# Kernel tuning notes

Measured on AMD Instinct MI355X. Metric: run time of the kernel, lower is better.

## Reference

```python
import jax, jax.numpy as jnp
import numpy as np

B, S, DM, H = 4, 1024, 1024, 16
D = DM // H  # attn_head_size = 64


def setup_inputs() -> dict:
    key = jax.random.key(0)
    ks = jax.random.split(key, 16)
    sc = 0.02
    return {
        "hidden_states": jax.random.normal(ks[0], (B, S, DM), jnp.float32),
        "wq": jax.random.normal(ks[1], (DM, DM), jnp.float32) * sc,
        "bq": jax.random.normal(ks[2], (DM,), jnp.float32) * sc,
        "wk": jax.random.normal(ks[3], (DM, DM), jnp.float32) * sc,
        "bk": jax.random.normal(ks[4], (DM,), jnp.float32) * sc,
        "wv": jax.random.normal(ks[5], (DM, DM), jnp.float32) * sc,
        "bv": jax.random.normal(ks[6], (DM,), jnp.float32) * sc,
        "wo": jax.random.normal(ks[7], (DM, DM), jnp.float32) * sc,
        "bo": jax.random.normal(ks[8], (DM,), jnp.float32) * sc,
        "wfq": jax.random.normal(ks[9], (DM, DM), jnp.float32) * sc,
        "bfq": jax.random.normal(ks[10], (DM,), jnp.float32) * sc,
        "wfg": jax.random.normal(ks[11], (DM, DM), jnp.float32) * sc,
        "bfg": jax.random.normal(ks[12], (DM,), jnp.float32) * sc,
        "up": jax.random.normal(ks[13], (H, 1, D), jnp.float32) * sc,
        "uz": jax.random.normal(ks[14], (H, 1, D), jnp.float32) * sc,
    }


def _split_heads(x):
    # [B, S, DM] -> [B, H, S, D]
    return x.reshape(x.shape[0], x.shape[1], H, D).transpose(0, 2, 1, 3)


def reference(hidden_states, wq, bq, wk, bk, wv, bv, wo, bo,
              wfq, bfq, wfg, bfg, up, uz):
    key_len = hidden_states.shape[1]
    mixed_q = hidden_states @ wq + bq  # [B, S, DM]
    mixed_k = hidden_states @ wk + bk
    mixed_v = hidden_states @ wv + bv

    # focus-attention Gaussian bias
    glo = jnp.mean(mixed_q, axis=1, keepdims=True)                      # [B, 1, DM]
    c = jnp.tanh((mixed_q @ wfq + bfq) + (glo @ wfg + bfg))             # [B, S, DM]
    c = _split_heads(c)                                                 # [B, H, S, D]
    p = jnp.sum(c * up[None], axis=-1)                                  # [B, H, S]
    z = jnp.sum(c * uz[None], axis=-1)                                  # [B, H, S]
    P = jax.nn.sigmoid(p) * key_len                                     # [B, H, S]
    Z = jax.nn.sigmoid(z) * key_len
    j = jnp.arange(key_len, dtype=P.dtype)                              # [S]
    # G[b,h,q,k] = -(k - P[b,h,q])^2 * 2 / Z[b,h,q]^2
    G = -((j[None, None, None, :] - P[..., None]) ** 2) * 2.0 / (Z[..., None] ** 2)

    q = _split_heads(mixed_q)
    k = _split_heads(mixed_k)
    v = _split_heads(mixed_v)

    scores = jnp.einsum("bhqd,bhkd->bhqk", q, k) / jnp.sqrt(jnp.float32(D))
    scores = scores + G
    probs = jax.nn.softmax(scores, axis=-1)  # dropout_prob = 0 -> no-op
    ctx = jnp.einsum("bhqk,bhkd->bhqd", probs, v)
    ctx = ctx.transpose(0, 2, 1, 3).reshape(ctx.shape[0], key_len, H * D)
    return ctx @ wo + bo
```

## Files before the change

kernel.cpp:

```cpp
#include <hip/hip_runtime.h>
#include <hip/hip_bf16.h>
#include <stdint.h>

#define DEV __device__ __forceinline__

typedef __attribute__((ext_vector_type(4))) float f32x4;
typedef __attribute__((ext_vector_type(8))) __bf16 bf16x8;
typedef __attribute__((ext_vector_type(4))) __bf16 bf16x4;
typedef __attribute__((ext_vector_type(4))) unsigned int uint4v;
typedef __attribute__((ext_vector_type(4))) int i32x4;

static constexpr int Bc = 4, Sc = 1024, DMc = 1024, Hc = 16, Dh = 64;
static constexpr int Mc = Bc * Sc;

DEV __bf16 f2b(float x) {
    unsigned u = __builtin_bit_cast(unsigned, x);
    unsigned r = (u + 0x7fffu + ((u >> 16) & 1u)) >> 16;
    return __builtin_bit_cast(__bf16, (unsigned short)r);
}
DEV float b2f(__bf16 x) {
    unsigned short s = __builtin_bit_cast(unsigned short, x);
    unsigned u = ((unsigned)s) << 16;
    return __builtin_bit_cast(float, u);
}
DEV unsigned cvt_pk_bf16(float a, float b) {
    unsigned r;
    asm("v_cvt_pk_bf16_f32 %0, %1, %2" : "=v"(r) : "v"(a), "v"(b));
    return r;
}
DEV void gload_lds16(const void* g, void* l) {
    __builtin_amdgcn_global_load_lds(
        (const __attribute__((address_space(1))) unsigned int*)g,
        (__attribute__((address_space(3))) unsigned int*)l,
        16, 0, 0);
}
DEV bf16x8 ldswz(const __bf16* base, int row, int cu) {
    const char* p = (const char*)base + row * 128 + (((cu) ^ (row & 7)) << 4);
    return *(const bf16x8*)p;
}

__global__ void k_cvt2(const float* __restrict__ hs, __bf16* __restrict__ hsb,
                       float* __restrict__ part0) {
    int sc = blockIdx.x, b = blockIdx.y, tid = threadIdx.x;
    int c0 = tid * 4;
    float4 s = {0.f, 0.f, 0.f, 0.f};
#pragma unroll
    for (int r = 0; r < 8; r++) {
        size_t row = (size_t)b * 1024 + sc * 8 + r;
        float4 v = *(const float4*)&hs[row * 1024 + c0];
        s.x += v.x; s.y += v.y; s.z += v.z; s.w += v.w;
        bf16x4 o = { f2b(v.x), f2b(v.y), f2b(v.z), f2b(v.w) };
        *(bf16x4*)&hsb[row * 1024 + c0] = o;
    }
    *(float4*)&part0[(size_t)(sc * 4 + b) * 1024 + c0] = s;
}

__global__ void k_tcvt5(const float* __restrict__ s0, const float* __restrict__ s1,
                        const float* __restrict__ s2, const float* __restrict__ s3,
                        const float* __restrict__ s4,
                        __bf16* __restrict__ d0, __bf16* __restrict__ d1,
                        __bf16* __restrict__ d2, __bf16* __restrict__ d3,
                        __bf16* __restrict__ d4, __bf16* __restrict__ wqb) {
    __shared__ float t[32][33];
    const float* in; __bf16* out;
    switch (blockIdx.z) {
        case 0: in = s0; out = d0; break;
        case 1: in = s1; out = d1; break;
        case 2: in = s2; out = d2; break;
        case 3: in = s3; out = d3; break;
        default: in = s4; out = d4; break;
    }
    int c0 = blockIdx.x * 32, r0 = blockIdx.y * 32;
    for (int j = 0; j < 4; j++) {
        float v = in[(size_t)(r0 + threadIdx.y + j * 8) * 1024 + c0 + threadIdx.x];
        t[threadIdx.y + j * 8][threadIdx.x] = v;
        if (blockIdx.z == 0)
            wqb[(size_t)(r0 + threadIdx.y + j * 8) * 1024 + c0 + threadIdx.x] = f2b(v);
    }
    __syncthreads();
    for (int j = 0; j < 4; j++)
        out[(size_t)(c0 + threadIdx.y + j * 8) * 1024 + r0 + threadIdx.x] = f2b(t[threadIdx.x][threadIdx.y + j * 8]);
}

template <int EPI, int BM>
__global__ __launch_bounds__(256) void k_gemm(
    const __bf16* __restrict__ A, const __bf16* __restrict__ Bt,
    const float* __restrict__ bias, void* __restrict__ Cout, int N, int K)
{
    constexpr int MF = BM / 32;
    constexpr int ACH = BM / 32;
    __shared__ __bf16 Al[2][BM * 64];
    __shared__ __bf16 Bl[2][128 * 64];
    const int bm = blockIdx.x, bn = blockIdx.y;
    const int tid = threadIdx.x, lane = tid & 63, wid = tid >> 6;
    const int l15 = lane & 15, lg = lane >> 4;
    const int qr = (wid >> 1) * (BM / 2), qc = (wid & 1) * 64;
    f32x4 acc[MF][4] = {};

    const __bf16* Ab = A + (size_t)bm * BM * K;
    const __bf16* Bb = Bt + (size_t)bn * 128 * K;

#pragma unroll
    for (int c = 0; c < ACH; c++) {
        int ch = c * 256 + tid, row = ch >> 3, cu = (ch & 7) ^ (row & 7);
        gload_lds16(&Ab[(size_t)row * K + cu * 8], &Al[0][ch * 8]);
    }
#pragma unroll
    for (int c = 0; c < 4; c++) {
        int ch = c * 256 + tid, row = ch >> 3, cu = (ch & 7) ^ (row & 7);
        gload_lds16(&Bb[(size_t)row * K + cu * 8], &Bl[0][ch * 8]);
    }
    asm volatile("s_waitcnt vmcnt(0)" ::: "memory");
    __builtin_amdgcn_s_barrier();

    int buf = 0;
    for (int t = 0; t < K / 64; t++) {
        if (t + 1 < K / 64) {
            int k0 = (t + 1) * 64;
#pragma unroll
            for (int c = 0; c < ACH; c++) {
                int ch = c * 256 + tid, row = ch >> 3, cu = (ch & 7) ^ (row & 7);
                gload_lds16(&Ab[(size_t)row * K + k0 + cu * 8], &Al[buf ^ 1][ch * 8]);
            }
#pragma unroll
            for (int c = 0; c < 4; c++) {
                int ch = c * 256 + tid, row = ch >> 3, cu = (ch & 7) ^ (row & 7);
                gload_lds16(&Bb[(size_t)row * K + k0 + cu * 8], &Bl[buf ^ 1][ch * 8]);
            }
        }
        bf16x8 af[MF][2], bfv[4][2];
#pragma unroll
        for (int m = 0; m < MF; m++)
#pragma unroll
            for (int ks = 0; ks < 2; ks++) af[m][ks] = ldswz(&Al[buf][0], qr + m * 16 + l15, ks * 4 + lg);
#pragma unroll
        for (int n = 0; n < 4; n++)
#pragma unroll
            for (int ks = 0; ks < 2; ks++) bfv[n][ks] = ldswz(&Bl[buf][0], qc + n * 16 + l15, ks * 4 + lg);
#pragma unroll
        for (int m = 0; m < MF; m++)
#pragma unroll
            for (int n = 0; n < 4; n++) {
                acc[m][n] = __builtin_amdgcn_mfma_f32_16x16x32_bf16(af[m][0], bfv[n][0], acc[m][n], 0, 0, 0);
                acc[m][n] = __builtin_amdgcn_mfma_f32_16x16x32_bf16(af[m][1], bfv[n][1], acc[m][n], 0, 0, 0);
            }
        asm volatile("s_waitcnt vmcnt(0)" ::: "memory");
        __builtin_amdgcn_s_barrier();
        buf ^= 1;
    }
#pragma unroll
    for (int m = 0; m < MF; m++) {
        int row_base = bm * BM + qr + m * 16 + lg * 4;
#pragma unroll
        for (int n = 0; n < 4; n++) {
            int col = bn * 128 + qc + n * 16 + l15;
            float bsum = bias ? bias[col] : 0.0f;
#pragma unroll
            for (int r = 0; r < 4; r++) {
                int row = row_base + r;
                float v = acc[m][n][r] + bsum;
                if constexpr (EPI == 2) ((float*)Cout)[(size_t)row * N + col] = v;
                else ((__bf16*)Cout)[(size_t)row * N + col] = f2b(v);
            }
        }
    }
}

__global__ __launch_bounds__(256) void k_qkvc(
    const __bf16* __restrict__ A, const __bf16* __restrict__ BtAll,
    const float* __restrict__ bq, const float* __restrict__ bk, const float* __restrict__ bv,
    const float* __restrict__ gt2, const float* __restrict__ up, const float* __restrict__ uz,
    __bf16* __restrict__ mq, __bf16* __restrict__ mk_, __bf16* __restrict__ mv_,
    float* __restrict__ Pf, float* __restrict__ Zf)
{
    constexpr int K = 1024;
    __shared__ __bf16 Al[2][128 * 64];
    __shared__ __bf16 Bl[2][128 * 64];
    const int bm = blockIdx.x, bn = blockIdx.y;
    const int tid = threadIdx.x, lane = tid & 63, wid = tid >> 6;
    const int l15 = lane & 15, lg = lane >> 4;
    const int qr = (wid >> 1) * 64, qc = (wid & 1) * 64;
    f32x4 acc[4][4] = {};

    const __bf16* Ab = A + (size_t)bm * 128 * K;
    const __bf16* Bb = BtAll + (size_t)bn * 128 * K;

#pragma unroll
    for (int c = 0; c < 4; c++) {
        int ch = c * 256 + tid, row = ch >> 3, cu = (ch & 7) ^ (row & 7);
        gload_lds16(&Ab[(size_t)row * K + cu * 8], &Al[0][ch * 8]);
        gload_lds16(&Bb[(size_t)row * K + cu * 8], &Bl[0][ch * 8]);
    }
    asm volatile("s_waitcnt vmcnt(0)" ::: "memory");
    __builtin_amdgcn_s_barrier();

    int buf = 0;
    for (int t = 0; t < 16; t++) {
        if (t < 15) {
            int k0 = (t + 1) * 64;
#pragma unroll
            for (int c = 0; c < 4; c++) {
                int ch = c * 256 + tid, row = ch >> 3, cu = (ch & 7) ^ (row & 7);
                gload_lds16(&Ab[(size_t)row * K + k0 + cu * 8], &Al[buf ^ 1][ch * 8]);
                gload_lds16(&Bb[(size_t)row * K + k0 + cu * 8], &Bl[buf ^ 1][ch * 8]);
            }
        }
        bf16x8 af[4][2], bfv[4][2];
#pragma unroll
        for (int m = 0; m < 4; m++)
#pragma unroll
            for (int ks = 0; ks < 2; ks++) af[m][ks] = ldswz(&Al[buf][0], qr + m * 16 + l15, ks * 4 + lg);
#pragma unroll
        for (int n = 0; n < 4; n++)
#pragma unroll
            for (int ks = 0; ks < 2; ks++) bfv[n][ks] = ldswz(&Bl[buf][0], qc + n * 16 + l15, ks * 4 + lg);
#pragma unroll
        for (int m = 0; m < 4; m++)
#pragma unroll
            for (int n = 0; n < 4; n++) {
                acc[m][n] = __builtin_amdgcn_mfma_f32_16x16x32_bf16(af[m][0], bfv[n][0], acc[m][n], 0, 0, 0);
                acc[m][n] = __builtin_amdgcn_mfma_f32_16x16x32_bf16(af[m][1], bfv[n][1], acc[m][n], 0, 0, 0);
            }
        asm volatile("s_waitcnt vmcnt(0)" ::: "memory");
        __builtin_amdgcn_s_barrier();
        buf ^= 1;
    }

    const int chunk = bn >> 3;
    if (chunk == 3) {
        const int h = (bn & 7) * 2 + (qc >> 6);
        float upv[4], uzv[4];
#pragma unroll
        for (int n = 0; n < 4; n++) {
            upv[n] = up[h * 64 + n * 16 + l15];
            uzv[n] = uz[h * 64 + n * 16 + l15];
        }
#pragma unroll
        for (int m = 0; m < 4; m++) {
            int row_base = bm * 128 + qr + m * 16 + lg * 4;
#pragma unroll
            for (int r = 0; r < 4; r++) {
                int row = row_base + r;
                float p = 0.f, z = 0.f;
#pragma unroll
                for (int n = 0; n < 4; n++) {
                    int col = (bn & 7) * 128 + qc + n * 16 + l15;
                    float cv = tanhf(acc[m][n][r] + gt2[(row >> 10) * 1024 + col]);
                    p += cv * upv[n];
                    z += cv * uzv[n];
                }
#pragma unroll
                for (int d = 1; d < 16; d <<= 1) {
                    p += __shfl_xor(p, d, 16);
                    z += __shfl_xor(z, d, 16);
                }
                if (l15 == 0) {
                    int bb = row >> 10, s = row & 1023;
                    Pf[((size_t)(bb * 16 + h)) * 1024 + s] = 1024.f / (1.f + __expf(-p));
                    Zf[((size_t)(bb * 16 + h)) * 1024 + s] = 1024.f / (1.f + __expf(-z));
                }
            }
        }
    } else {
        const float* bias = chunk == 0 ? bq : chunk == 1 ? bk : bv;
        __bf16* outp = chunk == 0 ? mq : chunk == 1 ? mk_ : mv_;
#pragma unroll
        for (int m = 0; m < 4; m++) {
            int row_base = bm * 128 + qr + m * 16 + lg * 4;
#pragma unroll
            for (int n = 0; n < 4; n++) {
                int col = (bn & 7) * 128 + qc + n * 16 + l15;
                float bsum = bias[col];
#pragma unroll
                for (int r = 0; r < 4; r++) {
                    int row = row_base + r;
                    outp[(size_t)row * 1024 + col] = f2b(acc[m][n][r] + bsum);
                }
            }
        }
    }
}

__global__ void k_glo2(const float* __restrict__ part0, const float* __restrict__ wq,
                       float* __restrict__ glo_part) {
    __shared__ float ghs_l[256];
    int tid = threadIdx.x, kc = blockIdx.y;
    {
        int bb = tid >> 6, kk = tid & 63, k = kc * 64 + kk;
        float s = 0.f;
        for (int sc = 0; sc < 128; sc++) s += part0[(size_t)(sc * 4 + bb) * 1024 + k];
        ghs_l[tid] = s * (1.0f / 1024.f);
    }
    __syncthreads();
    int n = blockIdx.x * 256 + tid;
    float a0 = 0, a1 = 0, a2 = 0, a3 = 0;
    for (int j = 0; j < 64; j++) {
        float w = wq[(size_t)(kc * 64 + j) * 1024 + n];
        a0 += ghs_l[j] * w; a1 += ghs_l[64 + j] * w; a2 += ghs_l[128 + j] * w; a3 += ghs_l[192 + j] * w;
    }
    glo_part[(kc * 4 + 0) * 1024 + n] = a0;
    glo_part[(kc * 4 + 1) * 1024 + n] = a1;
    glo_part[(kc * 4 + 2) * 1024 + n] = a2;
    glo_part[(kc * 4 + 3) * 1024 + n] = a3;
}
__global__ void k_gt2p(const float* __restrict__ glo_part, const float* __restrict__ bq,
                       const float* __restrict__ wfg, const float* __restrict__ wfq,
                       float* __restrict__ gt_part) {
    __shared__ float glo_l[256];
    int tid = threadIdx.x, kc = blockIdx.y;
    {
        int bb = tid >> 6, kk = tid & 63, k = kc * 64 + kk;
        float s = bq[k];
        for (int k2 = 0; k2 < 16; k2++) s += glo_part[(k2 * 4 + bb) * 1024 + k];
        glo_l[tid] = s;
    }
    __syncthreads();
    int n = blockIdx.x * 256 + tid;
    float a0 = 0, a1 = 0, a2 = 0, a3 = 0, t = 0;
    for (int j = 0; j < 64; j++) {
        int k = kc * 64 + j;
        float wg = wfg[(size_t)k * 1024 + n];
        float wf = wfq[(size_t)k * 1024 + n];
        a0 += glo_l[j] * wg; a1 += glo_l[64 + j] * wg; a2 += glo_l[128 + j] * wg; a3 += glo_l[192 + j] * wg;
        t += bq[k] * wf;
    }
    gt_part[(kc * 4 + 0) * 1024 + n] = a0 + t;
    gt_part[(kc * 4 + 1) * 1024 + n] = a1 + t;
    gt_part[(kc * 4 + 2) * 1024 + n] = a2 + t;
    gt_part[(kc * 4 + 3) * 1024 + n] = a3 + t;
}
__global__ void k_red_gt(const float* __restrict__ gt_part, const float* __restrict__ bfg,
                         const float* __restrict__ bfq, float* __restrict__ gt2) {
    int i = blockIdx.x * 256 + threadIdx.x;
    int b = i >> 10, n = i & 1023;
    float s = bfg[n] + bfq[n];
    for (int kc = 0; kc < 16; kc++) s += gt_part[(kc * 4 + b) * 1024 + n];
    gt2[i] = s;
}

__global__ __launch_bounds__(256) void k_vt(const __bf16* __restrict__ mv_, __bf16* __restrict__ vt) {
    __shared__ __bf16 tl[64][72];
    int sc = blockIdx.x, h = blockIdx.y, b = blockIdx.z;
    int tid = threadIdx.x;
#pragma unroll
    for (int i = 0; i < 2; i++) {
        int ch = i * 256 + tid, srow = ch >> 3, off = ch & 7;
        bf16x8 v = *(const bf16x8*)&mv_[((size_t)(b * 1024 + sc * 64 + srow)) * 1024 + h * 64 + off * 8];
        *(bf16x8*)&tl[srow][off * 8] = v;
    }
    __syncthreads();
#pragma unroll
    for (int i = 0; i < 2; i++) {
        int ch = i * 256 + tid, d = ch >> 3, offs = ch & 7;
        bf16x8 o;
#pragma unroll
        for (int j = 0; j < 8; j++) o[j] = tl[offs * 8 + j][d];
        *(bf16x8*)&vt[((size_t)((b * 16 + h) * 64 + d)) * 1024 + sc * 64 + offs * 8] = o;
    }
}

DEV bf16x8 ldfrag(const __bf16* base, int row, int colbyte) {
    const char* p = (const char*)base + (size_t)row * 128 + (colbyte ^ ((row & 7) << 4));
    return *(const bf16x8*)p;
}

__global__ __launch_bounds__(256) void k_attn(
    const __bf16* __restrict__ Q, const __bf16* __restrict__ Kx, const __bf16* __restrict__ Vt_g,
    const float* __restrict__ Pf, const float* __restrict__ Zf, __bf16* __restrict__ ctx)
{
    __shared__ __bf16 Kl[2][64 * 64];
    __shared__ __bf16 Vl[2][64 * 64];
    const int qt = blockIdx.x, h = blockIdx.y, b = blockIdx.z;
    const int tid = threadIdx.x, lane = tid & 63, wid = tid >> 6;
    const int l15 = lane & 15, lg = lane >> 4;
    const int qbase = qt * 128 + wid * 32;
    const size_t qoff = ((size_t)(b * Sc)) * DMc + h * Dh;

    bf16x8 qf[2][2];
#pragma unroll
    for (int qh = 0; qh < 2; qh++)
#pragma unroll
        for (int dh = 0; dh < 2; dh++)
            qf[qh][dh] = *(const bf16x8*)&Q[qoff + (size_t)(qbase + qh * 16 + l15) * DMc + dh * 32 + lg * 8];

    float Pr[2], Ar[2];
#pragma unroll
    for (int qh = 0; qh < 2; qh++) {
        int row = qbase + qh * 16 + l15;
        float pp = Pf[((size_t)(b * 16 + h)) * 1024 + row];
        float zz = Zf[((size_t)(b * 16 + h)) * 1024 + row];
        Pr[qh] = pp; Ar[qh] = 2.0f / (zz * zz);
    }
    float m[2] = {-1e30f, -1e30f}, l[2] = {0.f, 0.f};
    f32x4 oacc[2][4] = {};

    const __bf16* Kbase = Kx + qoff;
    const __bf16* Vbase = Vt_g + ((size_t)((b * 16 + h) * 64)) * 1024;

#pragma unroll
    for (int i = 0; i < 2; i++) {
        int ch = i * 256 + tid, row = ch >> 3, off = ch & 7;
        uint4v kv = *(const uint4v*)&Kbase[(size_t)row * DMc + off * 8];
        uint4v vv = *(const uint4v*)&Vbase[(size_t)row * 1024 + off * 8];
        *(uint4v*)((char*)&Kl[0][0] + row * 128 + ((off * 16) ^ ((row & 7) << 4))) = kv;
        *(uint4v*)((char*)&Vl[0][0] + row * 128 + ((off * 16) ^ ((row & 7) << 4))) = vv;
    }
    __syncthreads();

    for (int t = 0; t < 16; t++) {
        const int buf = t & 1;
        uint4v rk[2], rv[2];
        if (t < 15) {
#pragma unroll
            for (int i = 0; i < 2; i++) {
                int ch = i * 256 + tid, row = ch >> 3, off = ch & 7;
                rk[i] = *(const uint4v*)&Kbase[(size_t)((t + 1) * 64 + row) * DMc + off * 8];
                rv[i] = *(const uint4v*)&Vbase[(size_t)row * 1024 + (t + 1) * 64 + off * 8];
            }
        }

        f32x4 st[2][4];
        __builtin_amdgcn_s_setprio(1);
#pragma unroll
        for (int c = 0; c < 4; c++) {
            bf16x8 kb0 = ldfrag(&Kl[buf][0], c * 16 + l15, lg * 16);
            bf16x8 kb1 = ldfrag(&Kl[buf][0], c * 16 + l15, 64 + lg * 16);
#pragma unroll
            for (int qh = 0; qh < 2; qh++) {
                f32x4 a = {0.f, 0.f, 0.f, 0.f};
                a = __builtin_amdgcn_mfma_f32_16x16x32_bf16(kb0, qf[qh][0], a, 0, 0, 0);
                a = __builtin_amdgcn_mfma_f32_16x16x32_bf16(kb1, qf[qh][1], a, 0, 0, 0);
                st[qh][c] = a;
            }
        }
        __builtin_amdgcn_s_setprio(0);

        int pk[2][4][2];
#pragma unroll
        for (int qh = 0; qh < 2; qh++) {
            float s[16];
            float mx = -1e30f;
#pragma unroll
            for (int c = 0; c < 4; c++)
#pragma unroll
                for (int r = 0; r < 4; r++) {
                    float kidx = (float)(t * 64 + c * 16 + lg * 4 + r);
                    float dk = kidx - Pr[qh];
                    float v = st[qh][c][r] * 0.125f - dk * dk * Ar[qh];
                    s[c * 4 + r] = v;
                    mx = fmaxf(mx, v);
                }
            mx = fmaxf(mx, __shfl_xor(mx, 16, 64));
            mx = fmaxf(mx, __shfl_xor(mx, 32, 64));
            float nm = fmaxf(m[qh], mx);
            float sc_ = __expf(m[qh] - nm);
            m[qh] = nm;
            float rs = 0.f;
#pragma unroll
            for (int i = 0; i < 16; i++) { float p = __expf(s[i] - nm); s[i] = p; rs += p; }
            rs += __shfl_xor(rs, 16, 64);
            rs += __shfl_xor(rs, 32, 64);
            l[qh] = l[qh] * sc_ + rs;
#pragma unroll
            for (int c = 0; c < 4; c++) {
                pk[qh][c][0] = (int)cvt_pk_bf16(s[c * 4 + 0], s[c * 4 + 1]);
                pk[qh][c][1] = (int)cvt_pk_bf16(s[c * 4 + 2], s[c * 4 + 3]);
            }
#pragma unroll
            for (int r = 0; r < 4; r++) {
                float scr = __shfl(sc_, lg * 4 + r, 16);
#pragma unroll
                for (int dt = 0; dt < 4; dt++) oacc[qh][dt][r] *= scr;
            }
        }

        const int a0 = (((lg & 1) << 1) * 16 + l15) * 4;
        const int a1 = a0 + 64;
        const int selhi = lg >> 1;
#pragma unroll
        for (int kh = 0; kh < 2; kh++) {
            bf16x8 vb[4];
#pragma unroll
            for (int dt = 0; dt < 4; dt++) vb[dt] = ldfrag(&Vl[buf][0], dt * 16 + l15, kh * 64 + lg * 16);
#pragma unroll
            for (int qh = 0; qh < 2; qh++) {
                int w[4];
#pragma unroll
                for (int wi = 0; wi < 4; wi++) {
                    int addr = (wi < 2) ? a0 : a1;
                    int pr = wi & 1;
                    int va = __builtin_amdgcn_ds_bpermute(addr, pk[qh][kh * 2 + 0][pr]);
                    int vb2 = __builtin_amdgcn_ds_bpermute(addr, pk[qh][kh * 2 + 1][pr]);
                    w[wi] = selhi ? vb2 : va;
                }
                i32x4 wv = {w[0], w[1], w[2], w[3]};
                bf16x8 pa = __builtin_bit_cast(bf16x8, wv);
                __builtin_amdgcn_s_setprio(1);
#pragma unroll
                for (int dt = 0; dt < 4; dt++)
                    oacc[qh][dt] = __builtin_amdgcn_mfma_f32_16x16x32_bf16(pa, vb[dt], oacc[qh][dt], 0, 0, 0);
                __builtin_amdgcn_s_setprio(0);
            }
        }

        if (t < 15) {
#pragma unroll
            for (int i = 0; i < 2; i++) {
                int ch = i * 256 + tid, row = ch >> 3, off = ch & 7;
                *(uint4v*)((char*)&Kl[buf ^ 1][0] + row * 128 + ((off * 16) ^ ((row & 7) << 4))) = rk[i];
                *(uint4v*)((char*)&Vl[buf ^ 1][0] + row * 128 + ((off * 16) ^ ((row & 7) << 4))) = rv[i];
            }
        }
        __syncthreads();
    }

#pragma unroll
    for (int qh = 0; qh < 2; qh++) {
        float lr[4];
#pragma unroll
        for (int r = 0; r < 4; r++) lr[r] = __shfl(l[qh], lg * 4 + r, 16);
#pragma unroll
        for (int dt = 0; dt < 4; dt++)
#pragma unroll
            for (int r = 0; r < 4; r++) {
                int row = qbase + qh * 16 + lg * 4 + r;
                ctx[((size_t)(b * Sc) + row) * DMc + h * Dh + dt * 16 + l15] =
                    f2b(oacc[qh][dt][r] / lr[r]);
            }
    }
}

extern "C" void kernel_launch(void* const* d_in, const int* in_sizes, int n_in,
                              void* d_out, int out_size, void* d_ws, size_t ws_size,
                              hipStream_t stream) {
    const float* hs  = (const float*)d_in[0];
    const float* wq  = (const float*)d_in[1];
    const float* bq  = (const float*)d_in[2];
    const float* wk  = (const float*)d_in[3];
    const float* bk  = (const float*)d_in[4];
    const float* wv  = (const float*)d_in[5];
    const float* bv  = (const float*)d_in[6];
    const float* wo  = (const float*)d_in[7];
    const float* bo  = (const float*)d_in[8];
    const float* wfq = (const float*)d_in[9];
    const float* bfq = (const float*)d_in[10];
    const float* wfg = (const float*)d_in[11];
    const float* bfg = (const float*)d_in[12];
    const float* up  = (const float*)d_in[13];
    const float* uz  = (const float*)d_in[14];

    char* ws = (char*)d_ws;
    const size_t MB = 1ull << 20;
    __bf16* hsb   = (__bf16*)(ws);
    __bf16* BtAll = (__bf16*)(ws + 8 * MB);
    __bf16* wfqT  = (__bf16*)(ws + 16 * MB);
    __bf16* woT   = (__bf16*)(ws + 18 * MB);
    __bf16* mq    = (__bf16*)(ws + 20 * MB);
    __bf16* mk    = (__bf16*)(ws + 28 * MB);
    __bf16* mv    = (__bf16*)(ws + 36 * MB);
    __bf16* vt    = (__bf16*)(ws + 44 * MB);
    __bf16* ctxb  = (__bf16*)(ws);
    __bf16* wqb   = (__bf16*)(ws + 55 * MB);
    char* sm = ws + 52 * MB;
    float* Pf       = (float*)(sm);
    float* Zf       = (float*)(sm + (256 << 10));
    float* glo_part = (float*)(sm + (512 << 10));
    float* gt_part  = (float*)(sm + (768 << 10));
    float* gt2      = (float*)(sm + (1024 << 10));
    float* part0    = (float*)(ws + 57 * MB);

    k_cvt2<<<dim3(128, 4), 256, 0, stream>>>(hs, hsb, part0);
    k_tcvt5<<<dim3(32, 32, 5), dim3(32, 8), 0, stream>>>(
        wq, wk, wv, wfq, wo,
        BtAll, BtAll + 1048576, BtAll + 2097152, wfqT, woT, wqb);

    k_glo2<<<dim3(4, 16), 256, 0, stream>>>(part0, wq, glo_part);
    k_gt2p<<<dim3(4, 16), 256, 0, stream>>>(glo_part, bq, wfg, wfq, gt_part);
    k_red_gt<<<16, 256, 0, stream>>>(gt_part, bfg, bfq, gt2);

    k_gemm<0, 64><<<dim3(16, 8), 256, 0, stream>>>(wfqT, wqb, nullptr, BtAll + 3145728, DMc, DMc);

    k_qkvc<<<dim3(32, 32), 256, 0, stream>>>(hsb, BtAll, bq, bk, bv, gt2, up, uz,
                                             mq, mk, mv, Pf, Zf);

    k_vt<<<dim3(16, 16, 4), 256, 0, stream>>>(mv, vt);

    k_attn<<<dim3(8, 16, 4), 256, 0, stream>>>(mq, mk, vt, Pf, Zf, ctxb);

    k_gemm<2, 64><<<dim3(64, 8), 256, 0, stream>>>(ctxb, woT, bo, d_out, DMc, DMc);
}
```

Before: 180.3 us.

## Fuse V transpose into QKV GEMM epilogue and halve GEMM K-tile to 32

The QKV GEMM epilogue now writes the V chunk directly in transposed [b,h,d,s] layout, which removes the separate k_vt transpose kernel and its global round trip through the mv buffer. Separately, both GEMM kernels switch from 64-wide to 32-wide K stages with a new 4-unit XOR swizzle. This halves LDS per block, which may raise occupancy, but doubles the number of barrier/wait iterations. The transposed stores are 8-byte strided writes, which may coalesce poorly.

Measured after the change: 193.1 us. +7.1%, slower.

```diff
diff --git a/kernel.cpp b/kernel.cpp
--- a/kernel.cpp
+++ b/kernel.cpp
@@ -34,8 +34,8 @@
         (__attribute__((address_space(3))) unsigned int*)l,
         16, 0, 0);
 }
-DEV bf16x8 ldswz(const __bf16* base, int row, int cu) {
-    const char* p = (const char*)base + row * 128 + (((cu) ^ (row & 7)) << 4);
+DEV bf16x8 ldswz32(const __bf16* base, int row, int lg) {
+    const char* p = (const char*)base + row * 64 + (((lg) ^ ((row >> 1) & 3)) << 4);
     return *(const bf16x8*)p;
 }
 
@@ -88,9 +88,9 @@
     const float* __restrict__ bias, void* __restrict__ Cout, int N, int K)
 {
     constexpr int MF = BM / 32;
-    constexpr int ACH = BM / 32;
-    __shared__ __bf16 Al[2][BM * 64];
-    __shared__ __bf16 Bl[2][128 * 64];
+    constexpr int ACH = BM / 64;
+    __shared__ __bf16 Al[2][BM * 32];
+    __shared__ __bf16 Bl[2][128 * 32];
     const int bm = blockIdx.x, bn = blockIdx.y;
     const int tid = threadIdx.x, lane = tid & 63, wid = tid >> 6;
     const int l15 = lane & 15, lg = lane >> 4;
@@ -100,54 +100,42 @@
     const __bf16* Ab = A + (size_t)bm * BM * K;
     const __bf16* Bb = Bt + (size_t)bn * 128 * K;
 
-#pragma unroll
-    for (int c = 0; c < ACH; c++) {
-        int ch = c * 256 + tid, row = ch >> 3, cu = (ch & 7) ^ (row & 7);
-        gload_lds16(&Ab[(size_t)row * K + cu * 8], &Al[0][ch * 8]);
-    }
-#pragma unroll
-    for (int c = 0; c < 4; c++) {
-        int ch = c * 256 + tid, row = ch >> 3, cu = (ch & 7) ^ (row & 7);
-        gload_lds16(&Bb[(size_t)row * K + cu * 8], &Bl[0][ch * 8]);
-    }
+#define STAGE_G(k0, dst)                                                          \
+    _Pragma("unroll")                                                             \
+    for (int c = 0; c < ACH; c++) {                                               \
+        int ch = c * 256 + tid, row = ch >> 2, u = ch & 3;                        \
+        int su = u ^ ((row >> 1) & 3);                                            \
+        gload_lds16(&Ab[(size_t)row * K + (k0) + su * 8], &Al[dst][ch * 8]);      \
+    }                                                                             \
+    _Pragma("unroll")                                                             \
+    for (int c = 0; c < 2; c++) {                                                 \
+        int ch = c * 256 + tid, row = ch >> 2, u = ch & 3;                        \
+        int su = u ^ ((row >> 1) & 3);                                            \
+        gload_lds16(&Bb[(size_t)row * K + (k0) + su * 8], &Bl[dst][ch * 8]);      \
+    }
+
+    STAGE_G(0, 0);
     asm volatile("s_waitcnt vmcnt(0)" ::: "memory");
     __builtin_amdgcn_s_barrier();
 
     int buf = 0;
-    for (int t = 0; t < K / 64; t++) {
-        if (t + 1 < K / 64) {
-            int k0 = (t + 1) * 64;
-#pragma unroll
-            for (int c = 0; c < ACH; c++) {
-                int ch = c * 256 + tid, row = ch >> 3, cu = (ch & 7) ^ (row & 7);
-                gload_lds16(&Ab[(size_t)row * K + k0 + cu * 8], &Al[buf ^ 1][ch * 8]);
-            }
-#pragma unroll
-            for (int c = 0; c < 4; c++) {
-                int ch = c * 256 + tid, row = ch >> 3, cu = (ch & 7) ^ (row & 7);
-                gload_lds16(&Bb[(size_t)row * K + k0 + cu * 8], &Bl[buf ^ 1][ch * 8]);
-            }
-        }
-        bf16x8 af[MF][2], bfv[4][2];
+    for (int t = 0; t < K / 32; t++) {
+        if (t + 1 < K / 32) { STAGE_G((t + 1) * 32, buf ^ 1); }
+        bf16x8 af[MF], bfv[4];
+#pragma unroll
+        for (int m = 0; m < MF; m++) af[m] = ldswz32(&Al[buf][0], qr + m * 16 + l15, lg);
+#pragma unroll
+        for (int n = 0; n < 4; n++) bfv[n] = ldswz32(&Bl[buf][0], qc + n * 16 + l15, lg);
 #pragma unroll
         for (int m = 0; m < MF; m++)
 #pragma unroll
-            for (int ks = 0; ks < 2; ks++) af[m][ks] = ldswz(&Al[buf][0], qr + m * 16 + l15, ks * 4 + lg);
-#pragma unroll
-        for (int n = 0; n < 4; n++)
-#pragma unroll
-            for (int ks = 0; ks < 2; ks++) bfv[n][ks] = ldswz(&Bl[buf][0], qc + n * 16 + l15, ks * 4 + lg);
-#pragma unroll
-        for (int m = 0; m < MF; m++)
-#pragma unroll
-            for (int n = 0; n < 4; n++) {
-                acc[m][n] = __builtin_amdgcn_mfma_f32_16x16x32_bf16(af[m][0], bfv[n][0], acc[m][n], 0, 0, 0);
-                acc[m][n] = __builtin_amdgcn_mfma_f32_16x16x32_bf16(af[m][1], bfv[n][1], acc[m][n], 0, 0, 0);
-            }
+            for (int n = 0; n < 4; n++)
+                acc[m][n] = __builtin_amdgcn_mfma_f32_16x16x32_bf16(af[m], bfv[n], acc[m][n], 0, 0, 0);
         asm volatile("s_waitcnt vmcnt(0)" ::: "memory");
         __builtin_amdgcn_s_barrier();
         buf ^= 1;
     }
+#undef STAGE_G
 #pragma unroll
     for (int m = 0; m < MF; m++) {
         int row_base = bm * BM + qr + m * 16 + lg * 4;
@@ -170,12 +158,12 @@
     const __bf16* __restrict__ A, const __bf16* __restrict__ BtAll,
     const float* __restrict__ bq, const float* __restrict__ bk, const float* __restrict__ bv,
     const float* __restrict__ gt2, const float* __restrict__ up, const float* __restrict__ uz,
-    __bf16* __restrict__ mq, __bf16* __restrict__ mk_, __bf16* __restrict__ mv_,
+    __bf16* __restrict__ mq, __bf16* __restrict__ mk_, __bf16* __restrict__ vt,
     float* __restrict__ Pf, float* __restrict__ Zf)
 {
     constexpr int K = 1024;
-    __shared__ __bf16 Al[2][128 * 64];
-    __shared__ __bf16 Bl[2][128 * 64];
+    __shared__ __bf16 Al[2][128 * 32];
+    __shared__ __bf16 Bl[2][128 * 32];
     const int bm = blockIdx.x, bn = blockIdx.y;
     const int tid = threadIdx.x, lane = tid & 63, wid = tid >> 6;
     const int l15 = lane & 15, lg = lane >> 4;
@@ -185,46 +173,37 @@
     const __bf16* Ab = A + (size_t)bm * 128 * K;
     const __bf16* Bb = BtAll + (size_t)bn * 128 * K;
 
-#pragma unroll
-    for (int c = 0; c < 4; c++) {
-        int ch = c * 256 + tid, row = ch >> 3, cu = (ch & 7) ^ (row & 7);
-        gload_lds16(&Ab[(size_t)row * K + cu * 8], &Al[0][ch * 8]);
-        gload_lds16(&Bb[(size_t)row * K + cu * 8], &Bl[0][ch * 8]);
-    }
+#define STAGE_Q(k0, dst)                                                          \
+    _Pragma("unroll")                                                             \
+    for (int c = 0; c < 2; c++) {                                                 \
+        int ch = c * 256 + tid, row = ch >> 2, u = ch & 3;                        \
+        int su = u ^ ((row >> 1) & 3);                                            \
+        gload_lds16(&Ab[(size_t)row * K + (k0) + su * 8], &Al[dst][ch * 8]);      \
+        gload_lds16(&Bb[(size_t)row * K + (k0) + su * 8], &Bl[dst][ch * 8]);      \
+    }
+
+    STAGE_Q(0, 0);
     asm volatile("s_waitcnt vmcnt(0)" ::: "memory");
     __builtin_amdgcn_s_barrier();
 
     int buf = 0;
-    for (int t = 0; t < 16; t++) {
-        if (t < 15) {
-            int k0 = (t + 1) * 64;
-#pragma unroll
-            for (int c = 0; c < 4; c++) {
-                int ch = c * 256 + tid, row = ch >> 3, cu = (ch & 7) ^ (row & 7);
-                gload_lds16(&Ab[(size_t)row * K + k0 + cu * 8], &Al[buf ^ 1][ch * 8]);
-                gload_lds16(&Bb[(size_t)row * K + k0 + cu * 8], &Bl[buf ^ 1][ch * 8]);
-            }
-        }
-        bf16x8 af[4][2], bfv[4][2];
+    for (int t = 0; t < 32; t++) {
+        if (t < 31) { STAGE_Q((t + 1) * 32, buf ^ 1); }
+        bf16x8 af[4], bfv[4];
+#pragma unroll
+        for (int m = 0; m < 4; m++) af[m] = ldswz32(&Al[buf][0], qr + m * 16 + l15, lg);
+#pragma unroll
+        for (int n = 0; n < 4; n++) bfv[n] = ldswz32(&Bl[buf][0], qc + n * 16 + l15, lg);
 #pragma unroll
         for (int m = 0; m < 4; m++)
 #pragma unroll
-            for (int ks = 0; ks < 2; ks++) af[m][ks] = ldswz(&Al[buf][0], qr + m * 16 + l15, ks * 4 + lg);
-#pragma unroll
-        for (int n = 0; n < 4; n++)
-#pragma unroll
-            for (int ks = 0; ks < 2; ks++) bfv[n][ks] = ldswz(&Bl[buf][0], qc + n * 16 + l15, ks * 4 + lg);
-#pragma unroll
-        for (int m = 0; m < 4; m++)
-#pragma unroll
-            for (int n = 0; n < 4; n++) {
-                acc[m][n] = __builtin_amdgcn_mfma_f32_16x16x32_bf16(af[m][0], bfv[n][0], acc[m][n], 0, 0, 0);
-                acc[m][n] = __builtin_amdgcn_mfma_f32_16x16x32_bf16(af[m][1], bfv[n][1], acc[m][n], 0, 0, 0);
-            }
+            for (int n = 0; n < 4; n++)
+                acc[m][n] = __builtin_amdgcn_mfma_f32_16x16x32_bf16(af[m], bfv[n], acc[m][n], 0, 0, 0);
         asm volatile("s_waitcnt vmcnt(0)" ::: "memory");
         __builtin_amdgcn_s_barrier();
         buf ^= 1;
     }
+#undef STAGE_Q
 
     const int chunk = bn >> 3;
     if (chunk == 3) {
@@ -261,9 +240,24 @@
                 }
             }
         }
+    } else if (chunk == 2) {
+        const int b = bm >> 3;
+#pragma unroll
+        for (int m = 0; m < 4; m++) {
+            int s0 = (bm & 7) * 128 + qr + m * 16 + lg * 4;
+#pragma unroll
+            for (int n = 0; n < 4; n++) {
+                int col = (bn & 7) * 128 + qc + n * 16 + l15;
+                int h = col >> 6, d = col & 63;
+                float bsum = bv[col];
+                bf16x4 o = { f2b(acc[m][n][0] + bsum), f2b(acc[m][n][1] + bsum),
+                             f2b(acc[m][n][2] + bsum), f2b(acc[m][n][3] + bsum) };
+                *(bf16x4*)&vt[((size_t)((b * 16 + h) * 64 + d)) * 1024 + s0] = o;
+            }
+        }
     } else {
-        const float* bias = chunk == 0 ? bq : chunk == 1 ? bk : bv;
-        __bf16* outp = chunk == 0 ? mq : chunk == 1 ? mk_ : mv_;
+        const float* bias = chunk == 0 ? bq : bk;
+        __bf16* outp = chunk == 0 ? mq : mk_;
 #pragma unroll
         for (int m = 0; m < 4; m++) {
             int row_base = bm * 128 + qr + m * 16 + lg * 4;
@@ -336,27 +330,6 @@
     float s = bfg[n] + bfq[n];
     for (int kc = 0; kc < 16; kc++) s += gt_part[(kc * 4 + b) * 1024 + n];
     gt2[i] = s;
-}
-
-__global__ __launch_bounds__(256) void k_vt(const __bf16* __restrict__ mv_, __bf16* __restrict__ vt) {
-    __shared__ __bf16 tl[64][72];
-    int sc = blockIdx.x, h = blockIdx.y, b = blockIdx.z;
-    int tid = threadIdx.x;
-#pragma unroll
-    for (int i = 0; i < 2; i++) {
-        int ch = i * 256 + tid, srow = ch >> 3, off = ch & 7;
-        bf16x8 v = *(const bf16x8*)&mv_[((size_t)(b * 1024 + sc * 64 + srow)) * 1024 + h * 64 + off * 8];
-        *(bf16x8*)&tl[srow][off * 8] = v;
-    }
-    __syncthreads();
-#pragma unroll
-    for (int i = 0; i < 2; i++) {
-        int ch = i * 256 + tid, d = ch >> 3, offs = ch & 7;
-        bf16x8 o;
-#pragma unroll
-        for (int j = 0; j < 8; j++) o[j] = tl[offs * 8 + j][d];
-        *(bf16x8*)&vt[((size_t)((b * 16 + h) * 64 + d)) * 1024 + sc * 64 + offs * 8] = o;
-    }
 }
 
 DEV bf16x8 ldfrag(const __bf16* base, int row, int colbyte) {
@@ -557,8 +530,7 @@
     __bf16* woT   = (__bf16*)(ws + 18 * MB);
     __bf16* mq    = (__bf16*)(ws + 20 * MB);
     __bf16* mk    = (__bf16*)(ws + 28 * MB);
-    __bf16* mv    = (__bf16*)(ws + 36 * MB);
-    __bf16* vt    = (__bf16*)(ws + 44 * MB);
+    __bf16* vt    = (__bf16*)(ws + 36 * MB);
     __bf16* ctxb  = (__bf16*)(ws);
     __bf16* wqb   = (__bf16*)(ws + 55 * MB);
     char* sm = ws + 52 * MB;
@@ -581,9 +553,7 @@
     k_gemm<0, 64><<<dim3(16, 8), 256, 0, stream>>>(wfqT, wqb, nullptr, BtAll + 3145728, DMc, DMc);
 
     k_qkvc<<<dim3(32, 32), 256, 0, stream>>>(hsb, BtAll, bq, bk, bv, gt2, up, uz,
-                                             mq, mk, mv, Pf, Zf);
-
-    k_vt<<<dim3(16, 16, 4), 256, 0, stream>>>(mv, vt);
+                                             mq, mk, vt, Pf, Zf);
 
     k_attn<<<dim3(8, 16, 4), 256, 0, stream>>>(mq, mk, vt, Pf, Zf, ctxb);
 
```

## Write V transposed from QKV GEMM epilogue and double attention query tile

Applied to the files above, without the earlier changes.

The QKV projection epilogue now writes the V chunk directly in the per-head transposed layout that attention consumes, so the separate transpose kernel and its extra round trip through global memory go away. The attention kernel now gives each wave 64 query rows instead of 32, which halves the grid and reuses each K/V tile in shared memory across twice as many queries. The cost is more registers per thread for scores and accumulators, which may lower occupancy, and the grid shrinks to 256 blocks. The transposed V stores are 8-byte writes strided by 2 KB rows, which coalesce less well than the old row-major stores.

Result: slower. 186.2 us (+3.3%).

```diff
diff --git a/kernel.cpp b/kernel.cpp
--- a/kernel.cpp
+++ b/kernel.cpp
@@ -170,7 +170,7 @@
     const __bf16* __restrict__ A, const __bf16* __restrict__ BtAll,
     const float* __restrict__ bq, const float* __restrict__ bk, const float* __restrict__ bv,
     const float* __restrict__ gt2, const float* __restrict__ up, const float* __restrict__ uz,
-    __bf16* __restrict__ mq, __bf16* __restrict__ mk_, __bf16* __restrict__ mv_,
+    __bf16* __restrict__ mq, __bf16* __restrict__ mk_, __bf16* __restrict__ vt,
     float* __restrict__ Pf, float* __restrict__ Zf)
 {
     constexpr int K = 1024;
@@ -261,9 +261,24 @@
                 }
             }
         }
+    } else if (chunk == 2) {
+        const int b = bm >> 3;
+#pragma unroll
+        for (int m = 0; m < 4; m++) {
+            int s0 = (bm & 7) * 128 + qr + m * 16 + lg * 4;
+#pragma unroll
+            for (int n = 0; n < 4; n++) {
+                int col = (bn & 7) * 128 + qc + n * 16 + l15;
+                int h = col >> 6, d = col & 63;
+                float bsum = bv[col];
+                bf16x4 o = { f2b(acc[m][n][0] + bsum), f2b(acc[m][n][1] + bsum),
+                             f2b(acc[m][n][2] + bsum), f2b(acc[m][n][3] + bsum) };
+                *(bf16x4*)&vt[((size_t)((b * 16 + h) * 64 + d)) * 1024 + s0] = o;
+            }
+        }
     } else {
-        const float* bias = chunk == 0 ? bq : chunk == 1 ? bk : bv;
-        __bf16* outp = chunk == 0 ? mq : chunk == 1 ? mk_ : mv_;
+        const float* bias = chunk == 0 ? bq : bk;
+        __bf16* outp = chunk == 0 ? mq : mk_;
 #pragma unroll
         for (int m = 0; m < 4; m++) {
             int row_base = bm * 128 + qr + m * 16 + lg * 4;
@@ -338,27 +353,6 @@
     gt2[i] = s;
 }
 
-__global__ __launch_bounds__(256) void k_vt(const __bf16* __restrict__ mv_, __bf16* __restrict__ vt) {
-    __shared__ __bf16 tl[64][72];
-    int sc = blockIdx.x, h = blockIdx.y, b = blockIdx.z;
-    int tid = threadIdx.x;
-#pragma unroll
-    for (int i = 0; i < 2; i++) {
-        int ch = i * 256 + tid, srow = ch >> 3, off = ch & 7;
-        bf16x8 v = *(const bf16x8*)&mv_[((size_t)(b * 1024 + sc * 64 + srow)) * 1024 + h * 64 + off * 8];
-        *(bf16x8*)&tl[srow][off * 8] = v;
-    }
-    __syncthreads();
-#pragma unroll
-    for (int i = 0; i < 2; i++) {
-        int ch = i * 256 + tid, d = ch >> 3, offs = ch & 7;
-        bf16x8 o;
-#pragma unroll
-        for (int j = 0; j < 8; j++) o[j] = tl[offs * 8 + j][d];
-        *(bf16x8*)&vt[((size_t)((b * 16 + h) * 64 + d)) * 1024 + sc * 64 + offs * 8] = o;
-    }
-}
-
 DEV bf16x8 ldfrag(const __bf16* base, int row, int colbyte) {
     const char* p = (const char*)base + (size_t)row * 128 + (colbyte ^ ((row & 7) << 4));
     return *(const bf16x8*)p;
@@ -373,26 +367,28 @@
     const int qt = blockIdx.x, h = blockIdx.y, b = blockIdx.z;
     const int tid = threadIdx.x, lane = tid & 63, wid = tid >> 6;
     const int l15 = lane & 15, lg = lane >> 4;
-    const int qbase = qt * 128 + wid * 32;
+    const int qbase = qt * 256 + wid * 64;
     const size_t qoff = ((size_t)(b * Sc)) * DMc + h * Dh;
 
-    bf16x8 qf[2][2];
-#pragma unroll
-    for (int qh = 0; qh < 2; qh++)
+    bf16x8 qf[4][2];
+#pragma unroll
+    for (int qh = 0; qh < 4; qh++)
 #pragma unroll
         for (int dh = 0; dh < 2; dh++)
             qf[qh][dh] = *(const bf16x8*)&Q[qoff + (size_t)(qbase + qh * 16 + l15) * DMc + dh * 32 + lg * 8];
 
-    float Pr[2], Ar[2];
-#pragma unroll
-    for (int qh = 0; qh < 2; qh++) {
+    float Pr[4], Ar[4];
+#pragma unroll
+    for (int qh = 0; qh < 4; qh++) {
         int row = qbase + qh * 16 + l15;
         float pp = Pf[((size_t)(b * 16 + h)) * 1024 + row];
         float zz = Zf[((size_t)(b * 16 + h)) * 1024 + row];
         Pr[qh] = pp; Ar[qh] = 2.0f / (zz * zz);
     }
-    float m[2] = {-1e30f, -1e30f}, l[2] = {0.f, 0.f};
-    f32x4 oacc[2][4] = {};
+    float m[4], l[4];
+    f32x4 oacc[4][4] = {};
+#pragma unroll
+    for (int qh = 0; qh < 4; qh++) { m[qh] = -1e30f; l[qh] = 0.f; }
 
     const __bf16* Kbase = Kx + qoff;
     const __bf16* Vbase = Vt_g + ((size_t)((b * 16 + h) * 64)) * 1024;
@@ -419,14 +415,14 @@
             }
         }
 
-        f32x4 st[2][4];
+        f32x4 st[4][4];
         __builtin_amdgcn_s_setprio(1);
 #pragma unroll
         for (int c = 0; c < 4; c++) {
             bf16x8 kb0 = ldfrag(&Kl[buf][0], c * 16 + l15, lg * 16);
             bf16x8 kb1 = ldfrag(&Kl[buf][0], c * 16 + l15, 64 + lg * 16);
 #pragma unroll
-            for (int qh = 0; qh < 2; qh++) {
+            for (int qh = 0; qh < 4; qh++) {
                 f32x4 a = {0.f, 0.f, 0.f, 0.f};
                 a = __builtin_amdgcn_mfma_f32_16x16x32_bf16(kb0, qf[qh][0], a, 0, 0, 0);
                 a = __builtin_amdgcn_mfma_f32_16x16x32_bf16(kb1, qf[qh][1], a, 0, 0, 0);
@@ -435,9 +431,9 @@
         }
         __builtin_amdgcn_s_setprio(0);
 
-        int pk[2][4][2];
-#pragma unroll
-        for (int qh = 0; qh < 2; qh++) {
+        int pk[4][4][2];
+#pragma unroll
+        for (int qh = 0; qh < 4; qh++) {
             float s[16];
             float mx = -1e30f;
 #pragma unroll
@@ -483,7 +479,7 @@
 #pragma unroll
             for (int dt = 0; dt < 4; dt++) vb[dt] = ldfrag(&Vl[buf][0], dt * 16 + l15, kh * 64 + lg * 16);
 #pragma unroll
-            for (int qh = 0; qh < 2; qh++) {
+            for (int qh = 0; qh < 4; qh++) {
                 int w[4];
 #pragma unroll
                 for (int wi = 0; wi < 4; wi++) {
@@ -515,7 +511,7 @@
     }
 
 #pragma unroll
-    for (int qh = 0; qh < 2; qh++) {
+    for (int qh = 0; qh < 4; qh++) {
         float lr[4];
 #pragma unroll
         for (int r = 0; r < 4; r++) lr[r] = __shfl(l[qh], lg * 4 + r, 16);
@@ -557,8 +553,7 @@
     __bf16* woT   = (__bf16*)(ws + 18 * MB);
     __bf16* mq    = (__bf16*)(ws + 20 * MB);
     __bf16* mk    = (__bf16*)(ws + 28 * MB);
-    __bf16* mv    = (__bf16*)(ws + 36 * MB);
-    __bf16* vt    = (__bf16*)(ws + 44 * MB);
+    __bf16* vt    = (__bf16*)(ws + 36 * MB);
     __bf16* ctxb  = (__bf16*)(ws);
     __bf16* wqb   = (__bf16*)(ws + 55 * MB);
     char* sm = ws + 52 * MB;
@@ -581,11 +576,9 @@
     k_gemm<0, 64><<<dim3(16, 8), 256, 0, stream>>>(wfqT, wqb, nullptr, BtAll + 3145728, DMc, DMc);
 
     k_qkvc<<<dim3(32, 32), 256, 0, stream>>>(hsb, BtAll, bq, bk, bv, gt2, up, uz,
-                                             mq, mk, mv, Pf, Zf);
-
-    k_vt<<<dim3(16, 16, 4), 256, 0, stream>>>(mv, vt);
-
-    k_attn<<<dim3(8, 16, 4), 256, 0, stream>>>(mq, mk, vt, Pf, Zf, ctxb);
+                                             mq, mk, vt, Pf, Zf);
+
+    k_attn<<<dim3(4, 16, 4), 256, 0, stream>>>(mq, mk, vt, Pf, Zf, ctxb);
 
     k_gemm<2, 64><<<dim3(64, 8), 256, 0, stream>>>(ctxb, woT, bo, d_out, DMc, DMc);
 }
```
